# Performance work log

Measured on AMD Instinct MI355X. Metric: run time of the kernel, lower is better.

The kernel has to match this reference:

```python
import jax, jax.numpy as jnp
import numpy as np

M, K, N = 8192, 4096, 4096
INT8_MAX = 127.0


def setup_inputs() -> dict:
    key = jax.random.key(0)
    k1, k2, k3, k4 = jax.random.split(key, 4)
    inp = jax.random.normal(k1, (M, K), dtype=jnp.float32)
    # int8 weight [out_features, in_features]
    weight = jax.random.randint(k2, (N, K), -128, 128, dtype=jnp.int32).astype(jnp.int8)
    # per-output-channel dequant scale
    weight_scale = jax.random.uniform(k3, (N,), dtype=jnp.float32, minval=1e-3, maxval=1e-2)
    bias = jax.random.normal(k4, (N,), dtype=jnp.float32) * 0.01
    return {"input": inp, "weight": weight, "weight_scale": weight_scale, "bias": bias}


def reference(input, weight, weight_scale, bias):
    # Dynamic per-token symmetric int8 quantization (scaled_int8_quant with
    # scale=None, azp=None, symmetric=True): scale_a = max|x| / 127 per row.
    absmax = jnp.max(jnp.abs(input), axis=-1, keepdims=True)  # [M, 1]
    scale_a = jnp.where(absmax > 0, absmax / INT8_MAX, jnp.float32(1.0))
    q = jnp.clip(jnp.round(input / scale_a), -128, 127).astype(jnp.int8)  # [M, K]
    # and per-column (weight_scale) dequant, plus bias, in input dtype.
    acc = jnp.matmul(q.astype(jnp.int32), weight.T.astype(jnp.int32))  # [M, N] int32
    out = acc.astype(jnp.float32) * scale_a * weight_scale[None, :] + bias[None, :]
    return out.astype(input.dtype)
```

## Files before the change

kernel.cpp:

```cpp
#include <hip/hip_runtime.h>
#include <cstdint>

typedef __attribute__((ext_vector_type(4))) int int32x4;
typedef __attribute__((ext_vector_type(16))) int int32x16;

#define GLOBAL_AS __attribute__((address_space(1)))
#define LDS_AS    __attribute__((address_space(3)))

__global__ __launch_bounds__(256) void pack_w(
    const int* __restrict__ w32, uint32_t* __restrict__ w8_as_u32)
{
    const size_t i = (size_t)blockIdx.x * 256 + threadIdx.x;
    const int4 v = ((const int4*)w32)[i];
    w8_as_u32[i] = (v.x & 0xff) | ((v.y & 0xff) << 8) |
                   ((v.z & 0xff) << 16) | ((uint32_t)(v.w & 0xff) << 24);
}

__global__ __launch_bounds__(256) void quant_rows(
    const float* __restrict__ in, int8_t* __restrict__ q,
    float* __restrict__ sa, int K)
{
    const int row = blockIdx.x;
    const float4* rp = (const float4*)(in + (size_t)row * K);
    const int t = threadIdx.x;

    float amax = 0.f;
    float4 v[4];
#pragma unroll
    for (int i = 0; i < 4; ++i) {
        v[i] = rp[t + (i << 8)];
        amax = fmaxf(amax,
               fmaxf(fmaxf(fabsf(v[i].x), fabsf(v[i].y)),
                     fmaxf(fabsf(v[i].z), fabsf(v[i].w))));
    }

#pragma unroll
    for (int off = 32; off; off >>= 1)
        amax = fmaxf(amax, __shfl_xor(amax, off));
    __shared__ float smax[4];
    if ((t & 63) == 0) smax[t >> 6] = amax;
    __syncthreads();
    amax = fmaxf(fmaxf(smax[0], smax[1]), fmaxf(smax[2], smax[3]));

    const float scale = (amax > 0.f) ? (amax / 127.f) : 1.f;
    if (t == 0) sa[row] = scale;
    const float rs = 1.f / scale;

    int* qrow = (int*)(q + (size_t)row * K);
#pragma unroll
    for (int i = 0; i < 4; ++i) {
        int a = __float2int_rn(v[i].x * rs);
        int b = __float2int_rn(v[i].y * rs);
        int c = __float2int_rn(v[i].z * rs);
        int d = __float2int_rn(v[i].w * rs);
        a = max(-128, min(127, a));
        b = max(-128, min(127, b));
        c = max(-128, min(127, c));
        d = max(-128, min(127, d));
        qrow[t + (i << 8)] = (a & 0xff) | ((b & 0xff) << 8) |
                             ((c & 0xff) << 16) | ((d & 0xff) << 24);
    }
}

__device__ __forceinline__ void async_load16(const int8_t* g, int8_t* lds) {
    __builtin_amdgcn_global_load_lds((const GLOBAL_AS char*)g,
                                     (LDS_AS char*)lds, 16, 0, 0);
}

__global__ __launch_bounds__(256, 1) void w8a8_gemm(
    const int8_t* __restrict__ Aq, const int8_t* __restrict__ W,
    const float* __restrict__ sa, const float* __restrict__ wsc,
    const float* __restrict__ bias, float* __restrict__ out,
    int M, int N, int K)
{
    __shared__ int8_t lds[4 * 32768];

    const int MB = M >> 8, NB = N >> 8;
    int bm, bn;
    if (MB == 32 && NB == 16) {
        const int x = blockIdx.x & 7, i = blockIdx.x >> 3;
        bm = ((x >> 1) << 3) + (i >> 3);
        bn = ((x & 1) << 3) + (i & 7);
    } else {
        const int cpx = gridDim.x >> 3;
        const int wg = (blockIdx.x & 7) * cpx + (blockIdx.x >> 3);
        bm = wg / NB; bn = wg % NB;
    }

    const int t = threadIdx.x;
    const int lane = t & 63, wid = t >> 6;
    const int wr = wid >> 1, wc = wid & 1;
    const int l31 = lane & 31, h = lane >> 5;
    const int pswz = ((lane >> 1) ^ (lane >> 3)) & 3;

    const int srow = t >> 2;
    const int scol = (((t & 3) ^ ((t >> 3) & 3) ^ ((t >> 5) & 3)) << 4);
    const int8_t* gA = Aq + ((size_t)bm * 256 + srow) * (size_t)K + scol;
    const int8_t* gB = W  + ((size_t)bn * 256 + srow) * (size_t)K + scol;
    const size_t rstep = (size_t)64 * K;
    const size_t hstep = (size_t)128 * K;
    int8_t* ldsw = &lds[t * 16];

    auto stage_tile = [&](int slot, int kbyte) {
#pragma unroll
        for (int c = 0; c < 4; ++c) {
            const int8_t* s0 = (c < 2 ? gA : gB) + (size_t)(c & 1) * hstep + kbyte;
            int8_t* d0 = ldsw + slot * 32768 + (c >> 1) * 16384 + (c & 1) * 8192;
            async_load16(s0, d0);
            async_load16(s0 + rstep, d0 + 4096);
        }
    };

    const int aoff = wr * 8192 + l31 * 64;
    const int boff = 16384 + wc * 8192 + l31 * 64;
    const int cs0 = ((0 + h) ^ pswz) << 4;
    const int cs1 = ((2 + h) ^ pswz) << 4;

    int32x16 acc[4][4];
#pragma unroll
    for (int m = 0; m < 4; ++m)
#pragma unroll
        for (int n = 0; n < 4; ++n)
#pragma unroll
            for (int rgi = 0; rgi < 16; ++rgi)
                acc[m][n][rgi] = 0;

    const int NT = K >> 6;

    stage_tile(0, 0);
    stage_tile(1, 64);
    asm volatile("s_waitcnt vmcnt(8)" ::: "memory");
    asm volatile("s_barrier" ::: "memory");

    for (int g = 0; g < NT; ++g) {
        const int rbase = (g & 3) * 32768;

        if (g + 2 < NT) stage_tile((g + 2) & 3, (g + 2) << 6);

        int32x4 a0[4], b0[4], a1[4], b1[4];
#pragma unroll
        for (int m = 0; m < 4; ++m)
            a0[m] = *(const int32x4*)&lds[rbase + aoff + m * 2048 + cs0];
#pragma unroll
        for (int n = 0; n < 4; ++n)
            b0[n] = *(const int32x4*)&lds[rbase + boff + n * 2048 + cs0];
#pragma unroll
        for (int m = 0; m < 4; ++m)
            a1[m] = *(const int32x4*)&lds[rbase + aoff + m * 2048 + cs1];
#pragma unroll
        for (int n = 0; n < 4; ++n)
            b1[n] = *(const int32x4*)&lds[rbase + boff + n * 2048 + cs1];

#pragma unroll
        for (int m = 0; m < 4; ++m)
#pragma unroll
            for (int n = 0; n < 4; ++n)
                acc[m][n] = __builtin_amdgcn_mfma_i32_32x32x32_i8(
                    a0[m], b0[n], acc[m][n], 0, 0, 0);
#pragma unroll
        for (int m = 0; m < 4; ++m)
#pragma unroll
            for (int n = 0; n < 4; ++n)
                acc[m][n] = __builtin_amdgcn_mfma_i32_32x32x32_i8(
                    a1[m], b1[n], acc[m][n], 0, 0, 0);

        if (g < NT - 2)
            asm volatile("s_waitcnt vmcnt(8)" ::: "memory");
        else
            asm volatile("s_waitcnt vmcnt(0)" ::: "memory");
        asm volatile("s_barrier" ::: "memory");
    }

    const int col0 = bn * 256 + wc * 128 + l31;
    const int row00 = bm * 256 + wr * 128 + 4 * h;

#pragma unroll
    for (int m = 0; m < 4; ++m) {
        float sv[16];
#pragma unroll
        for (int rgi = 0; rgi < 16; ++rgi)
            sv[rgi] = sa[row00 + m * 32 + (rgi & 3) + 8 * (rgi >> 2)];
#pragma unroll
        for (int n = 0; n < 4; ++n) {
            const int col = col0 + n * 32;
            const float wn = wsc[col];
            const float bb = bias[col];
#pragma unroll
            for (int rgi = 0; rgi < 16; ++rgi) {
                const int row = row00 + m * 32 + (rgi & 3) + 8 * (rgi >> 2);
                out[(size_t)row * N + col] =
                    (float)acc[m][n][rgi] * sv[rgi] * wn + bb;
            }
        }
    }
}

extern "C" void kernel_launch(void* const* d_in, const int* in_sizes, int n_in,
                              void* d_out, int out_size, void* d_ws, size_t ws_size,
                              hipStream_t stream) {
    const float* inp  = (const float*)d_in[0];
    const int*   w32  = (const int*)d_in[1];
    const float* wsc  = (const float*)d_in[2];
    const float* bias = (const float*)d_in[3];
    float* out = (float*)d_out;

    const int N = in_sizes[2];
    const int K = in_sizes[1] / N;
    const int M = in_sizes[0] / K;

    int8_t* q  = (int8_t*)d_ws;
    float*  sa = (float*)((char*)d_ws + (size_t)M * K);
    int8_t* w8 = (int8_t*)((char*)d_ws + (size_t)M * K + (size_t)M * 4 + 256);

    const size_t nw4 = ((size_t)N * K) / 4;
    pack_w<<<(int)(nw4 / 256), 256, 0, stream>>>(w32, (uint32_t*)w8);

    quant_rows<<<M, 256, 0, stream>>>(inp, q, sa, K);

    const int nwg = (M / 256) * (N / 256);
    w8a8_gemm<<<nwg, 256, 0, stream>>>(q, w8, sa, wsc, bias, out, M, N, K);
}
```

Measured before the change: 201.8 us.

## Reorganize LDS tile layout to lane-contiguous fragments and simplify block mapping

Changes the global-to-LDS staging pattern so that each 16-byte MFMA fragment a lane needs sits contiguously at lane*16, with the two k-halves 1024 bytes apart. This removes the XOR swizzle and avoids bank conflicts on ds_read_b128 without extra address math. It also moves the first half of the fragment reads ahead of the async stage issue and replaces the hand-tuned 8x8 block remap with a generic XCD-chunked mapping. The cost is that global reads become 32-row strided 16-byte chunks per wave instead of 64-byte row runs, and L2 locality for the block mapping may change.

Result: slower. 208.2 us (+3.2%).

```diff
diff --git a/kernel.cpp b/kernel.cpp
--- a/kernel.cpp
+++ b/kernel.cpp
@@ -75,46 +75,35 @@
 {
     __shared__ int8_t lds[4 * 32768];
 
-    const int MB = M >> 8, NB = N >> 8;
-    int bm, bn;
-    if (MB == 32 && NB == 16) {
-        const int x = blockIdx.x & 7, i = blockIdx.x >> 3;
-        bm = ((x >> 1) << 3) + (i >> 3);
-        bn = ((x & 1) << 3) + (i & 7);
-    } else {
-        const int cpx = gridDim.x >> 3;
-        const int wg = (blockIdx.x & 7) * cpx + (blockIdx.x >> 3);
-        bm = wg / NB; bn = wg % NB;
-    }
+    const int NB = N >> 8;
+    const int nwg = gridDim.x;
+    const int cpx = nwg >> 3;
+    const int wg = (blockIdx.x & 7) * cpx + (blockIdx.x >> 3);
+    const int bm = wg / NB, bn = wg % NB;
 
     const int t = threadIdx.x;
     const int lane = t & 63, wid = t >> 6;
     const int wr = wid >> 1, wc = wid & 1;
     const int l31 = lane & 31, h = lane >> 5;
-    const int pswz = ((lane >> 1) ^ (lane >> 3)) & 3;
-
-    const int srow = t >> 2;
-    const int scol = (((t & 3) ^ ((t >> 3) & 3) ^ ((t >> 5) & 3)) << 4);
+
+    const int srow = ((t >> 7) & 1) * 32 + (t & 31);
+    const int scol = ((((t >> 6) & 1) * 2 + ((t >> 5) & 1)) << 4);
     const int8_t* gA = Aq + ((size_t)bm * 256 + srow) * (size_t)K + scol;
     const int8_t* gB = W  + ((size_t)bn * 256 + srow) * (size_t)K + scol;
-    const size_t rstep = (size_t)64 * K;
-    const size_t hstep = (size_t)128 * K;
+    const size_t cstep = (size_t)64 * K;
     int8_t* ldsw = &lds[t * 16];
 
     auto stage_tile = [&](int slot, int kbyte) {
+        int8_t* d = ldsw + slot * 32768;
 #pragma unroll
         for (int c = 0; c < 4; ++c) {
-            const int8_t* s0 = (c < 2 ? gA : gB) + (size_t)(c & 1) * hstep + kbyte;
-            int8_t* d0 = ldsw + slot * 32768 + (c >> 1) * 16384 + (c & 1) * 8192;
-            async_load16(s0, d0);
-            async_load16(s0 + rstep, d0 + 4096);
+            async_load16(gA + c * cstep + kbyte, d + c * 4096);
+            async_load16(gB + c * cstep + kbyte, d + 16384 + c * 4096);
         }
     };
 
-    const int aoff = wr * 8192 + l31 * 64;
-    const int boff = 16384 + wc * 8192 + l31 * 64;
-    const int cs0 = ((0 + h) ^ pswz) << 4;
-    const int cs1 = ((2 + h) ^ pswz) << 4;
+    const int aoff = wr * 8192 + lane * 16;
+    const int boff = 16384 + wc * 8192 + lane * 16;
 
     int32x16 acc[4][4];
 #pragma unroll
@@ -135,21 +124,22 @@
     for (int g = 0; g < NT; ++g) {
         const int rbase = (g & 3) * 32768;
 
+        int32x4 a0[4], b0[4], a1[4], b1[4];
+#pragma unroll
+        for (int m = 0; m < 4; ++m)
+            a0[m] = *(const int32x4*)&lds[rbase + aoff + m * 2048];
+#pragma unroll
+        for (int n = 0; n < 4; ++n)
+            b0[n] = *(const int32x4*)&lds[rbase + boff + n * 2048];
+
         if (g + 2 < NT) stage_tile((g + 2) & 3, (g + 2) << 6);
 
-        int32x4 a0[4], b0[4], a1[4], b1[4];
-#pragma unroll
-        for (int m = 0; m < 4; ++m)
-            a0[m] = *(const int32x4*)&lds[rbase + aoff + m * 2048 + cs0];
+#pragma unroll
+        for (int m = 0; m < 4; ++m)
+            a1[m] = *(const int32x4*)&lds[rbase + aoff + m * 2048 + 1024];
 #pragma unroll
         for (int n = 0; n < 4; ++n)
-            b0[n] = *(const int32x4*)&lds[rbase + boff + n * 2048 + cs0];
-#pragma unroll
-        for (int m = 0; m < 4; ++m)
-            a1[m] = *(const int32x4*)&lds[rbase + aoff + m * 2048 + cs1];
-#pragma unroll
-        for (int n = 0; n < 4; ++n)
-            b1[n] = *(const int32x4*)&lds[rbase + boff + n * 2048 + cs1];
+            b1[n] = *(const int32x4*)&lds[rbase + boff + n * 2048 + 1024];
 
 #pragma unroll
         for (int m = 0; m < 4; ++m)
```
